# Kernel optimization log

Measured on AMD Instinct MI355X. Metric: run time of the kernel, lower is better.

The kernel has to match this reference:

```python
import jax, jax.numpy as jnp
import numpy as np

N_NODES = 100000
N_EDGES = 1600000
IN_DIM = 128
OUT_DIM = 64
NEG_SLOPE = 0.01  # torch F.leaky_relu default


def setup_inputs() -> dict:
    key = jax.random.key(0)
    k1, k2, k3, k4, k5 = jax.random.split(key, 5)
    h = jax.random.normal(k1, (N_NODES, IN_DIM), dtype=jnp.float32)
    src = jax.random.randint(k2, (N_EDGES,), 0, N_NODES, dtype=jnp.int32)
    dst = jax.random.randint(k3, (N_EDGES,), 0, N_NODES, dtype=jnp.int32)
    # xavier_normal with relu gain, as in reset_parameters
    gain = float(np.sqrt(2.0))
    fc_std = gain * np.sqrt(2.0 / (IN_DIM + OUT_DIM))
    at_std = gain * np.sqrt(2.0 / (2 * OUT_DIM + 1))
    fc_w = jax.random.normal(k4, (OUT_DIM, IN_DIM), dtype=jnp.float32) * fc_std
    attn_w = jax.random.normal(k5, (2 * OUT_DIM,), dtype=jnp.float32) * at_std
    return {"h": h, "src": src, "dst": dst, "fc_w": fc_w, "attn_w": attn_w}


def reference(h, src, dst, fc_w, attn_w):
    n = h.shape[0]
    d = fc_w.shape[0]
    z = h @ fc_w.T                                  # [N, D]
    # per-edge attention logit: attn_fc(concat(z_src, z_dst)) split into two dots
    a_src = z @ attn_w[:d]                          # [N]
    a_dst = z @ attn_w[d:]                          # [N]
    e = a_src[src] + a_dst[dst]                     # [E]
    e = jnp.where(e >= 0, e, NEG_SLOPE * e)         # leaky_relu
    # segment softmax over incoming edges of each dst node
    e_max = jax.ops.segment_max(e, dst, num_segments=n)   # [N]
    ex = jnp.exp(e - e_max[dst])                    # [E]
    denom = jax.ops.segment_sum(ex, dst, num_segments=n)  # [N]
    alpha = ex / denom[dst]                         # [E]
    # weighted scatter-sum of source features
    h_out = jax.ops.segment_sum(alpha[:, None] * z[src], dst, num_segments=n)
    return h_out
```

## Files before the change

kernel.cpp:

```cpp
#include <hip/hip_runtime.h>

#define D 64
#define IN 128
#define NEG_SLOPE 0.01f

#define NSLICE 32
#define SUBPS  32
#define NSUB   1024
#define EPB_A  3328
#define EPT_A  13
#define HALF   49
#define CAP2   1152
#define CAP_S  53248
#define CAP_SUB 2304

using f32x4  = __attribute__((ext_vector_type(4))) float;
using bf16x8 = __attribute__((ext_vector_type(8))) short;
using u16x8  = __attribute__((ext_vector_type(8))) unsigned short;

__device__ __forceinline__ short f2bf(float f) {
    unsigned u = __float_as_uint(f);
    u = u + 0x7FFFu + ((u >> 16) & 1u);
    return (short)(u >> 16);
}
__device__ __forceinline__ float bf2f(unsigned short u) {
    return __uint_as_float((unsigned)u << 16);
}
__device__ __forceinline__ int mdiv(int n, unsigned M) {
    return (int)__umulhi((unsigned)n, M);
}

__global__ __launch_bounds__(256) void k_partA_proj(
    const int* __restrict__ src, const int* __restrict__ dst,
    int* __restrict__ slice_cur, int* __restrict__ partA,
    int n_edges, int nps1, unsigned M1, int n_partA,
    const float* __restrict__ h, const float* __restrict__ fc_w,
    const float* __restrict__ attn_w,
    unsigned short* __restrict__ zb, float* __restrict__ a_src, float* __restrict__ a_dst,
    int n_nodes)
{
    __shared__ int smem[4352];

    if (blockIdx.x < n_partA) {
        int* loff  = smem;
        int* lbase = smem + 40;
        int* lcur  = smem + 80;
        int* lsort = smem + 128;
        const int tid = threadIdx.x;
        const int e0 = blockIdx.x * EPB_A;
        const int e1 = min(e0 + EPB_A, n_edges);

        if (tid < NSLICE) { loff[tid] = 0; lcur[tid] = 0; }
        __syncthreads();

        int myp[EPT_A], mysl[EPT_A];
        #pragma unroll
        for (int j = 0; j < EPT_A; ++j) {
            int i = e0 + j * 256 + tid;
            mysl[j] = -1;
            if (i < e1) {
                int d = dst[i], s = src[i];
                int sl = mdiv(d, M1);
                mysl[j] = sl;
                myp[j]  = s | ((d - sl * nps1) << 17);
                atomicAdd(&loff[sl], 1);
            }
        }
        __syncthreads();
        if (tid < NSLICE) {
            int v = loff[tid];
            int sc = v;
            #pragma unroll
            for (int o = 1; o < NSLICE; o <<= 1) {
                int t2 = __shfl_up(sc, o, 64);
                if (tid >= o) sc += t2;
            }
            loff[tid] = sc - v;
            if (tid == NSLICE - 1) loff[NSLICE] = sc;
        }
        __syncthreads();
        if (tid < NSLICE)
            lbase[tid] = tid * CAP_S + atomicAdd(&slice_cur[tid * 16], loff[tid + 1] - loff[tid]);
        #pragma unroll
        for (int j = 0; j < EPT_A; ++j)
            if (mysl[j] >= 0) {
                int r = atomicAdd(&lcur[mysl[j]], 1);
                lsort[loff[mysl[j]] + r] = myp[j];
            }
        __syncthreads();
        for (int s = 0; s < NSLICE; ++s) {
            int b = loff[s], e = loff[s + 1], gb = lbase[s];
            int lim = (s + 1) * CAP_S;
            for (int i = b + tid; i < e; i += 256) {
                int pos = gb + (i - b);
                if (pos < lim) partA[pos] = lsort[i];
            }
        }
        return;
    }

    float* zst = (float*)smem;
    const int wid  = threadIdx.x >> 6;
    const int lane = threadIdx.x & 63;
    const int g16  = lane >> 4;
    const int l16  = lane & 15;

    bf16x8 bfrag[4][4];
    #pragma unroll
    for (int t = 0; t < 4; ++t) {
        const float* wrow = fc_w + (size_t)(t * 16 + l16) * IN + g16 * 8;
        #pragma unroll
        for (int ks = 0; ks < 4; ++ks) {
            f32x4 w0 = *(const f32x4*)(wrow + ks * 32);
            f32x4 w1 = *(const f32x4*)(wrow + ks * 32 + 4);
            bf16x8 b;
            b[0] = f2bf(w0[0]); b[1] = f2bf(w0[1]); b[2] = f2bf(w0[2]); b[3] = f2bf(w0[3]);
            b[4] = f2bf(w1[0]); b[5] = f2bf(w1[1]); b[6] = f2bf(w1[2]); b[7] = f2bf(w1[3]);
            bfrag[t][ks] = b;
        }
    }

    float awx[4], awy[4];
    #pragma unroll
    for (int t = 0; t < 4; ++t) {
        awx[t] = attn_w[t * 16 + l16];
        awy[t] = attn_w[D + t * 16 + l16];
    }

    const int grp0 = (blockIdx.x - n_partA) * 16 + wid * 4;
    #pragma unroll
    for (int it = 0; it < 4; ++it) {
        const int gb = (grp0 + it) * 16;
        if (gb >= n_nodes) break;

        const float* hrow = h + (size_t)(gb + l16) * IN + g16 * 8;
        bf16x8 afrag[4];
        #pragma unroll
        for (int ks = 0; ks < 4; ++ks) {
            f32x4 h0 = *(const f32x4*)(hrow + ks * 32);
            f32x4 h1 = *(const f32x4*)(hrow + ks * 32 + 4);
            bf16x8 a;
            a[0] = f2bf(h0[0]); a[1] = f2bf(h0[1]); a[2] = f2bf(h0[2]); a[3] = f2bf(h0[3]);
            a[4] = f2bf(h1[0]); a[5] = f2bf(h1[1]); a[6] = f2bf(h1[2]); a[7] = f2bf(h1[3]);
            afrag[ks] = a;
        }

        f32x4 acc[4] = {f32x4{0,0,0,0}, f32x4{0,0,0,0}, f32x4{0,0,0,0}, f32x4{0,0,0,0}};
        #pragma unroll
        for (int t = 0; t < 4; ++t)
            #pragma unroll
            for (int ks = 0; ks < 4; ++ks)
                acc[t] = __builtin_amdgcn_mfma_f32_16x16x32_bf16(
                    afrag[ks], bfrag[t][ks], acc[t], 0, 0, 0);

        #pragma unroll
        for (int t = 0; t < 4; ++t)
            #pragma unroll
            for (int r = 0; r < 4; ++r)
                zst[wid * 1088 + (g16 * 4 + r) * 68 + t * 16 + l16] = acc[t][r];

        const int rrow = lane >> 2;
        const int rcol = (lane & 3) * 16;
        const float* zr0 = &zst[wid * 1088 + rrow * 68 + rcol];
        f32x4 v0 = *(const f32x4*)(zr0);
        f32x4 v1 = *(const f32x4*)(zr0 + 4);
        f32x4 v2 = *(const f32x4*)(zr0 + 8);
        f32x4 v3 = *(const f32x4*)(zr0 + 12);
        u16x8 p0, p1;
        p0[0] = (unsigned short)f2bf(v0[0]); p0[1] = (unsigned short)f2bf(v0[1]);
        p0[2] = (unsigned short)f2bf(v0[2]); p0[3] = (unsigned short)f2bf(v0[3]);
        p0[4] = (unsigned short)f2bf(v1[0]); p0[5] = (unsigned short)f2bf(v1[1]);
        p0[6] = (unsigned short)f2bf(v1[2]); p0[7] = (unsigned short)f2bf(v1[3]);
        p1[0] = (unsigned short)f2bf(v2[0]); p1[1] = (unsigned short)f2bf(v2[1]);
        p1[2] = (unsigned short)f2bf(v2[2]); p1[3] = (unsigned short)f2bf(v2[3]);
        p1[4] = (unsigned short)f2bf(v3[0]); p1[5] = (unsigned short)f2bf(v3[1]);
        p1[6] = (unsigned short)f2bf(v3[2]); p1[7] = (unsigned short)f2bf(v3[3]);
        *(u16x8*)&zb[(size_t)(gb + rrow) * D + rcol]     = p0;
        *(u16x8*)&zb[(size_t)(gb + rrow) * D + rcol + 8] = p1;

        #pragma unroll
        for (int r = 0; r < 4; ++r) {
            float as = acc[0][r] * awx[0] + acc[1][r] * awx[1]
                     + acc[2][r] * awx[2] + acc[3][r] * awx[3];
            float ad = acc[0][r] * awy[0] + acc[1][r] * awy[1]
                     + acc[2][r] * awy[2] + acc[3][r] * awy[3];
            #pragma unroll
            for (int o = 1; o < 16; o <<= 1) {
                as += __shfl_xor(as, o, 64);
                ad += __shfl_xor(ad, o, 64);
            }
            if (l16 == 0) {
                a_src[gb + g16 * 4 + r] = as;
                a_dst[gb + g16 * 4 + r] = ad;
            }
        }
    }
}

__global__ __launch_bounds__(256) void k_partB(
    const int* __restrict__ partA, const int* __restrict__ slice_cur,
    int* __restrict__ sub_cur, int* __restrict__ part2, int nps2, unsigned M2)
{
    __shared__ int loff[SUBPS + 1], lbase[SUBPS], lcur[SUBPS];
    __shared__ int lsort[2048];
    const int tid   = threadIdx.x;
    const int slice = blockIdx.x >> 5;
    const int bid   = blockIdx.x & 31;
    const int s0   = slice * CAP_S;
    const int cntS = min(slice_cur[slice * 16], CAP_S);
    const int chunk = (cntS + 31) >> 5;
    int c0 = s0 + bid * chunk;
    int c1 = min(c0 + chunk, s0 + cntS);

    for (int r0 = c0; r0 < c1; r0 += 2048) {
        int r1 = min(r0 + 2048, c1);
        if (tid < SUBPS) { loff[tid] = 0; lcur[tid] = 0; }
        __syncthreads();
        int myp[8], mysb[8];
        #pragma unroll
        for (int j = 0; j < 8; ++j) {
            int i = r0 + j * 256 + tid;
            mysb[j] = -1;
            if (i < r1) {
                int p = partA[i];
                int dloc = p >> 17;
                int sb = mdiv(dloc, M2);
                mysb[j] = sb;
                myp[j]  = (p & 0x1FFFF) | ((dloc - sb * nps2) << 17);
                atomicAdd(&loff[sb], 1);
            }
        }
        __syncthreads();
        if (tid < SUBPS) {
            int v = loff[tid];
            int sc = v;
            #pragma unroll
            for (int o = 1; o < SUBPS; o <<= 1) {
                int t2 = __shfl_up(sc, o, 64);
                if (tid >= o) sc += t2;
            }
            loff[tid] = sc - v;
            if (tid == SUBPS - 1) loff[SUBPS] = sc;
        }
        __syncthreads();
        if (tid < SUBPS) {
            int sub = slice * SUBPS + tid;
            lbase[tid] = sub * CAP_SUB + atomicAdd(&sub_cur[sub], loff[tid + 1] - loff[tid]);
        }
        #pragma unroll
        for (int j = 0; j < 8; ++j)
            if (mysb[j] >= 0) {
                int r = atomicAdd(&lcur[mysb[j]], 1);
                lsort[loff[mysb[j]] + r] = myp[j];
            }
        __syncthreads();
        for (int s = 0; s < SUBPS; ++s) {
            int b = loff[s], e = loff[s + 1], gb = lbase[s];
            int lim = (slice * SUBPS + s + 1) * CAP_SUB;
            for (int i = b + tid; i < e; i += 256) {
                int pos = gb + (i - b);
                if (pos < lim) part2[pos] = lsort[i];
            }
        }
        __syncthreads();
    }
}

__global__ __launch_bounds__(256) void k_fused(
    const int* __restrict__ part2, const int* __restrict__ sub_cur,
    const float* __restrict__ a_src, const float* __restrict__ a_dst,
    const u16x8* __restrict__ zb8, float4* __restrict__ out4,
    int n_nodes, int nps2)
{
    __shared__ int   sdeg[56], scur[56];
    __shared__ float sden[56];
    __shared__ int   soff[65];
    __shared__ int   sstage[CAP_SUB];
    __shared__ int2  sedge[CAP2];

    const int tid  = threadIdx.x;
    const int sub  = blockIdx.x >> 1;
    const int half = blockIdx.x & 1;
    const int nb0  = sub * nps2;
    if (nb0 >= n_nodes) return;
    const int nn   = min(nps2, n_nodes - nb0);
    const int lo   = half * HALF;
    const int hi   = min(nn, lo + HALF);
    const int nloc = hi - lo;
    if (nloc <= 0) return;
    const int s0  = sub * CAP_SUB;
    const int cnt = min(sub_cur[sub], CAP_SUB);

    for (int i = tid; i < 56; i += 256) { sdeg[i] = 0; scur[i] = 0; sden[i] = 0.f; }
    __syncthreads();

    for (int i = tid; i < cnt; i += 256) {
        int p = part2[s0 + i];
        sstage[i] = p;
        int local = p >> 17;
        if (local >= lo && local < hi) atomicAdd(&sdeg[local - lo], 1);
    }
    __syncthreads();

    if (tid < 64) {
        int v = (tid < nloc) ? sdeg[tid] : 0;
        int sc = v;
        #pragma unroll
        for (int o = 1; o < 64; o <<= 1) {
            int t2 = __shfl_up(sc, o, 64);
            if (tid >= o) sc += t2;
        }
        soff[tid + 1] = sc;
        if (tid == 0) soff[0] = 0;
    }
    __syncthreads();

    const bool fits = (soff[nloc] <= CAP2);

    if (fits) {
        for (int i = tid; i < cnt; i += 256) {
            int p = sstage[i];
            int local = p >> 17;
            if (local >= lo && local < hi) {
                int l2 = local - lo;
                int s = p & 0x1FFFF;
                int pos = soff[l2] + atomicAdd(&scur[l2], 1);
                float e = a_src[s] + a_dst[nb0 + local];
                e = (e >= 0.f) ? e : NEG_SLOPE * e;
                float ex = __expf(e);
                sedge[pos] = make_int2(s << 3, __float_as_int(ex));
                atomicAdd(&sden[l2], ex);
            }
        }
    }
    __syncthreads();

    if (fits) {
        const int group = tid >> 3;
        const int l8    = tid & 7;
        for (int n = group; n < nloc; n += 32) {
            int beg = soff[n], deg = sdeg[n];
            f32x4 a0 = {0.f,0.f,0.f,0.f}, a1 = {0.f,0.f,0.f,0.f};
            for (int i = 0; i < deg; ++i) {
                int2 me = sedge[beg + i];
                float w = __int_as_float(me.y);
                u16x8 zr = zb8[(size_t)me.x + l8];
                a0[0] = fmaf(w, bf2f(zr[0]), a0[0]);
                a0[1] = fmaf(w, bf2f(zr[1]), a0[1]);
                a0[2] = fmaf(w, bf2f(zr[2]), a0[2]);
                a0[3] = fmaf(w, bf2f(zr[3]), a0[3]);
                a1[0] = fmaf(w, bf2f(zr[4]), a1[0]);
                a1[1] = fmaf(w, bf2f(zr[5]), a1[1]);
                a1[2] = fmaf(w, bf2f(zr[6]), a1[2]);
                a1[3] = fmaf(w, bf2f(zr[7]), a1[3]);
            }
            float inv = (deg > 0) ? 1.f / sden[n] : 0.f;
            out4[(size_t)(nb0 + lo + n) * 16 + l8 * 2] =
                make_float4(a0[0] * inv, a0[1] * inv, a0[2] * inv, a0[3] * inv);
            out4[(size_t)(nb0 + lo + n) * 16 + l8 * 2 + 1] =
                make_float4(a1[0] * inv, a1[1] * inv, a1[2] * inv, a1[3] * inv);
        }
    } else {
        const ushort4* zb4 = (const ushort4*)zb8;
        const int wave = tid >> 6, lane = tid & 63, l16 = lane & 15;
        for (int n = wave; n < nloc; n += 4) {
            int deg = 0;
            float adn = a_dst[nb0 + lo + n];
            float dsum = 0.f;
            float4 acc = make_float4(0.f, 0.f, 0.f, 0.f);
            for (int c = 0; c < cnt; c += 64) {
                int j = c + lane;
                float ex = 0.f;
                if (j < cnt) {
                    int p = sstage[j];
                    if ((p >> 17) == lo + n) {
                        float e = a_src[p & 0x1FFFF] + adn;
                        e = (e >= 0.f) ? e : NEG_SLOPE * e;
                        ex = __expf(e);
                        ++deg;
                    }
                }
                float exs = ex;
                #pragma unroll
                for (int o = 32; o > 0; o >>= 1) exs += __shfl_xor(exs, o, 64);
                dsum += exs;
            }
            #pragma unroll
            for (int o = 32; o > 0; o >>= 1) deg += __shfl_xor(deg, o, 64);
            for (int j = 0; j < cnt; ++j) {
                int p = sstage[j];
                if ((p >> 17) == lo + n) {
                    int s = p & 0x1FFFF;
                    float e = a_src[s] + adn;
                    e = (e >= 0.f) ? e : NEG_SLOPE * e;
                    float w = __expf(e);
                    if (lane < 16) {
                        ushort4 zr = zb4[(size_t)(s << 4) + l16];
                        acc.x = fmaf(w, bf2f(zr.x), acc.x);
                        acc.y = fmaf(w, bf2f(zr.y), acc.y);
                        acc.z = fmaf(w, bf2f(zr.z), acc.z);
                        acc.w = fmaf(w, bf2f(zr.w), acc.w);
                    }
                }
            }
            #pragma unroll
            for (int o = 16; o <= 32; o <<= 1) {
                acc.x += __shfl_xor(acc.x, o, 64);
                acc.y += __shfl_xor(acc.y, o, 64);
                acc.z += __shfl_xor(acc.z, o, 64);
                acc.w += __shfl_xor(acc.w, o, 64);
            }
            if (lane < 16) {
                float inv = (deg > 0) ? 1.f / dsum : 0.f;
                out4[(size_t)(nb0 + lo + n) * 16 + l16] =
                    make_float4(acc.x * inv, acc.y * inv, acc.z * inv, acc.w * inv);
            }
        }
    }
}

extern "C" void kernel_launch(void* const* d_in, const int* in_sizes, int n_in,
                              void* d_out, int out_size, void* d_ws, size_t ws_size,
                              hipStream_t stream) {
    const float* h      = (const float*)d_in[0];
    const int*   src    = (const int*)d_in[1];
    const int*   dst    = (const int*)d_in[2];
    const float* fc_w   = (const float*)d_in[3];
    const float* attn_w = (const float*)d_in[4];

    const int n_nodes = in_sizes[0] / IN;
    const int n_edges = in_sizes[1];
    float* out = (float*)d_out;

    const int nps2 = (n_nodes + NSUB - 1) / NSUB;
    const int nps1 = nps2 * SUBPS;
    const int nba  = (n_edges + EPB_A - 1) / EPB_A;
    const int n_proj = (n_nodes + 255) / 256;
    const unsigned M1 = (unsigned)((0x100000000ULL + nps1 - 1) / (unsigned)nps1);
    const unsigned M2 = (unsigned)((0x100000000ULL + nps2 - 1) / (unsigned)nps2);

    char* p = (char*)d_ws;
    unsigned short* zb = (unsigned short*)p; p += (size_t)n_nodes * D * sizeof(unsigned short);
    int*   partA     = (int*)p;   p += (size_t)NSLICE * CAP_S * sizeof(int);
    int*   part2     = (int*)p;   p += (size_t)NSUB * CAP_SUB * sizeof(int);
    float* a_src     = (float*)p; p += (size_t)n_nodes * sizeof(float);
    float* a_dst     = (float*)p; p += (size_t)n_nodes * sizeof(float);
    int*   slice_cur = (int*)p;   p += NSLICE * 16 * sizeof(int);
    int*   sub_cur   = (int*)p;   p += NSUB * sizeof(int);

    hipMemsetAsync(slice_cur, 0, (NSLICE * 16 + NSUB) * sizeof(int), stream);

    k_partA_proj<<<dim3(nba + n_proj), dim3(256), 0, stream>>>(
        src, dst, slice_cur, partA, n_edges, nps1, M1, nba,
        h, fc_w, attn_w, zb, a_src, a_dst, n_nodes);
    k_partB<<<dim3(NSLICE * 32), dim3(256), 0, stream>>>(
        partA, slice_cur, sub_cur, part2, nps2, M2);
    k_fused<<<dim3(NSUB * 2), dim3(256), 0, stream>>>(
        part2, sub_cur, a_src, a_dst, (const u16x8*)zb, (float4*)out, n_nodes, nps2);
}
```

Baseline: 95.57 us.

## Move projection GEMM to run alongside second partition pass; vectorize first pass loads

The node projection blocks are now co-launched with the second-level bucketing pass instead of the first-level pass, so the first partition kernel runs alone with smaller 2048-edge blocks. Those blocks load src/dst with int4 vector loads. The aim is better load balance between the two bucketing passes and the projection work, and fewer, wider memory transactions for the edge reads. More blocks in the first pass means more global atomics on the slice counters.

```diff
diff --git a/kernel.cpp b/kernel.cpp
--- a/kernel.cpp
+++ b/kernel.cpp
@@ -7,8 +7,7 @@
 #define NSLICE 32
 #define SUBPS  32
 #define NSUB   1024
-#define EPB_A  3328
-#define EPT_A  13
+#define EPB_A  2048
 #define HALF   49
 #define CAP2   1152
 #define CAP_S  53248
@@ -30,10 +29,80 @@
     return (int)__umulhi((unsigned)n, M);
 }
 
-__global__ __launch_bounds__(256) void k_partA_proj(
+__global__ __launch_bounds__(256) void k_partA(
     const int* __restrict__ src, const int* __restrict__ dst,
     int* __restrict__ slice_cur, int* __restrict__ partA,
-    int n_edges, int nps1, unsigned M1, int n_partA,
+    int n_edges, int nps1, unsigned M1)
+{
+    __shared__ int loff[NSLICE + 1], lbase[NSLICE], lcur[NSLICE];
+    __shared__ int lsort[EPB_A];
+    const int tid = threadIdx.x;
+    const int e0 = blockIdx.x * EPB_A;
+    const int e1 = min(e0 + EPB_A, n_edges);
+
+    if (tid < NSLICE) { loff[tid] = 0; lcur[tid] = 0; }
+    __syncthreads();
+
+    const int4* dst4 = (const int4*)dst;
+    const int4* src4 = (const int4*)src;
+    int myp[8], mysl[8];
+    #pragma unroll
+    for (int c = 0; c < 2; ++c) {
+        int b4 = (e0 >> 2) + c * 256 + tid;
+        bool v4 = (b4 * 4 < e1);
+        int4 d4 = v4 ? dst4[b4] : make_int4(0, 0, 0, 0);
+        int4 s4 = v4 ? src4[b4] : make_int4(0, 0, 0, 0);
+        const int* dp = (const int*)&d4;
+        const int* sp = (const int*)&s4;
+        #pragma unroll
+        for (int k = 0; k < 4; ++k) {
+            int j = c * 4 + k;
+            mysl[j] = -1;
+            int idx = b4 * 4 + k;
+            if (v4 && idx < e1) {
+                int d = dp[k], s = sp[k];
+                int sl = mdiv(d, M1);
+                mysl[j] = sl;
+                myp[j]  = s | ((d - sl * nps1) << 17);
+                atomicAdd(&loff[sl], 1);
+            }
+        }
+    }
+    __syncthreads();
+    if (tid < NSLICE) {
+        int v = loff[tid];
+        int sc = v;
+        #pragma unroll
+        for (int o = 1; o < NSLICE; o <<= 1) {
+            int t2 = __shfl_up(sc, o, 64);
+            if (tid >= o) sc += t2;
+        }
+        loff[tid] = sc - v;
+        if (tid == NSLICE - 1) loff[NSLICE] = sc;
+    }
+    __syncthreads();
+    if (tid < NSLICE)
+        lbase[tid] = tid * CAP_S + atomicAdd(&slice_cur[tid * 16], loff[tid + 1] - loff[tid]);
+    #pragma unroll
+    for (int j = 0; j < 8; ++j)
+        if (mysl[j] >= 0) {
+            int r = atomicAdd(&lcur[mysl[j]], 1);
+            lsort[loff[mysl[j]] + r] = myp[j];
+        }
+    __syncthreads();
+    for (int s = 0; s < NSLICE; ++s) {
+        int b = loff[s], e = loff[s + 1], gb = lbase[s];
+        int lim = (s + 1) * CAP_S;
+        for (int i = b + tid; i < e; i += 256) {
+            int pos = gb + (i - b);
+            if (pos < lim) partA[pos] = lsort[i];
+        }
+    }
+}
+
+__global__ __launch_bounds__(256) void k_partB_proj(
+    const int* __restrict__ partA, const int* __restrict__ slice_cur,
+    int* __restrict__ sub_cur, int* __restrict__ part2, int nps2, unsigned M2,
     const float* __restrict__ h, const float* __restrict__ fc_w,
     const float* __restrict__ attn_w,
     unsigned short* __restrict__ zb, float* __restrict__ a_src, float* __restrict__ a_dst,
@@ -41,60 +110,71 @@
 {
     __shared__ int smem[4352];
 
-    if (blockIdx.x < n_partA) {
+    if (blockIdx.x < NSUB) {
         int* loff  = smem;
         int* lbase = smem + 40;
         int* lcur  = smem + 80;
         int* lsort = smem + 128;
-        const int tid = threadIdx.x;
-        const int e0 = blockIdx.x * EPB_A;
-        const int e1 = min(e0 + EPB_A, n_edges);
-
-        if (tid < NSLICE) { loff[tid] = 0; lcur[tid] = 0; }
-        __syncthreads();
-
-        int myp[EPT_A], mysl[EPT_A];
-        #pragma unroll
-        for (int j = 0; j < EPT_A; ++j) {
-            int i = e0 + j * 256 + tid;
-            mysl[j] = -1;
-            if (i < e1) {
-                int d = dst[i], s = src[i];
-                int sl = mdiv(d, M1);
-                mysl[j] = sl;
-                myp[j]  = s | ((d - sl * nps1) << 17);
-                atomicAdd(&loff[sl], 1);
-            }
-        }
-        __syncthreads();
-        if (tid < NSLICE) {
-            int v = loff[tid];
-            int sc = v;
-            #pragma unroll
-            for (int o = 1; o < NSLICE; o <<= 1) {
-                int t2 = __shfl_up(sc, o, 64);
-                if (tid >= o) sc += t2;
-            }
-            loff[tid] = sc - v;
-            if (tid == NSLICE - 1) loff[NSLICE] = sc;
-        }
-        __syncthreads();
-        if (tid < NSLICE)
-            lbase[tid] = tid * CAP_S + atomicAdd(&slice_cur[tid * 16], loff[tid + 1] - loff[tid]);
-        #pragma unroll
-        for (int j = 0; j < EPT_A; ++j)
-            if (mysl[j] >= 0) {
-                int r = atomicAdd(&lcur[mysl[j]], 1);
-                lsort[loff[mysl[j]] + r] = myp[j];
-            }
-        __syncthreads();
-        for (int s = 0; s < NSLICE; ++s) {
-            int b = loff[s], e = loff[s + 1], gb = lbase[s];
-            int lim = (s + 1) * CAP_S;
-            for (int i = b + tid; i < e; i += 256) {
-                int pos = gb + (i - b);
-                if (pos < lim) partA[pos] = lsort[i];
-            }
+        const int tid   = threadIdx.x;
+        const int slice = blockIdx.x >> 5;
+        const int bid   = blockIdx.x & 31;
+        const int s0   = slice * CAP_S;
+        const int cntS = min(slice_cur[slice * 16], CAP_S);
+        const int chunk = (cntS + 31) >> 5;
+        int c0 = s0 + bid * chunk;
+        int c1 = min(c0 + chunk, s0 + cntS);
+
+        for (int r0 = c0; r0 < c1; r0 += 2048) {
+            int r1 = min(r0 + 2048, c1);
+            if (tid < SUBPS) { loff[tid] = 0; lcur[tid] = 0; }
+            __syncthreads();
+            int myp[8], mysb[8];
+            #pragma unroll
+            for (int j = 0; j < 8; ++j) {
+                int i = r0 + j * 256 + tid;
+                mysb[j] = -1;
+                if (i < r1) {
+                    int p = partA[i];
+                    int dloc = p >> 17;
+                    int sb = mdiv(dloc, M2);
+                    mysb[j] = sb;
+                    myp[j]  = (p & 0x1FFFF) | ((dloc - sb * nps2) << 17);
+                    atomicAdd(&loff[sb], 1);
+                }
+            }
+            __syncthreads();
+            if (tid < SUBPS) {
+                int v = loff[tid];
+                int sc = v;
+                #pragma unroll
+                for (int o = 1; o < SUBPS; o <<= 1) {
+                    int t2 = __shfl_up(sc, o, 64);
+                    if (tid >= o) sc += t2;
+                }
+                loff[tid] = sc - v;
+                if (tid == SUBPS - 1) loff[SUBPS] = sc;
+            }
+            __syncthreads();
+            if (tid < SUBPS) {
+                int sub = slice * SUBPS + tid;
+                lbase[tid] = sub * CAP_SUB + atomicAdd(&sub_cur[sub], loff[tid + 1] - loff[tid]);
+            }
+            #pragma unroll
+            for (int j = 0; j < 8; ++j)
+                if (mysb[j] >= 0) {
+                    int r = atomicAdd(&lcur[mysb[j]], 1);
+                    lsort[loff[mysb[j]] + r] = myp[j];
+                }
+            __syncthreads();
+            for (int s = 0; s < SUBPS; ++s) {
+                int b = loff[s], e = loff[s + 1], gb = lbase[s];
+                int lim = (slice * SUBPS + s + 1) * CAP_SUB;
+                for (int i = b + tid; i < e; i += 256) {
+                    int pos = gb + (i - b);
+                    if (pos < lim) part2[pos] = lsort[i];
+                }
+            }
+            __syncthreads();
         }
         return;
     }
@@ -127,7 +207,7 @@
         awy[t] = attn_w[D + t * 16 + l16];
     }
 
-    const int grp0 = (blockIdx.x - n_partA) * 16 + wid * 4;
+    const int grp0 = (blockIdx.x - NSUB) * 16 + wid * 4;
     #pragma unroll
     for (int it = 0; it < 4; ++it) {
         const int gb = (grp0 + it) * 16;
@@ -194,75 +274,6 @@
                 a_dst[gb + g16 * 4 + r] = ad;
             }
         }
-    }
-}
-
-__global__ __launch_bounds__(256) void k_partB(
-    const int* __restrict__ partA, const int* __restrict__ slice_cur,
-    int* __restrict__ sub_cur, int* __restrict__ part2, int nps2, unsigned M2)
-{
-    __shared__ int loff[SUBPS + 1], lbase[SUBPS], lcur[SUBPS];
-    __shared__ int lsort[2048];
-    const int tid   = threadIdx.x;
-    const int slice = blockIdx.x >> 5;
-    const int bid   = blockIdx.x & 31;
-    const int s0   = slice * CAP_S;
-    const int cntS = min(slice_cur[slice * 16], CAP_S);
-    const int chunk = (cntS + 31) >> 5;
-    int c0 = s0 + bid * chunk;
-    int c1 = min(c0 + chunk, s0 + cntS);
-
-    for (int r0 = c0; r0 < c1; r0 += 2048) {
-        int r1 = min(r0 + 2048, c1);
-        if (tid < SUBPS) { loff[tid] = 0; lcur[tid] = 0; }
-        __syncthreads();
-        int myp[8], mysb[8];
-        #pragma unroll
-        for (int j = 0; j < 8; ++j) {
-            int i = r0 + j * 256 + tid;
-            mysb[j] = -1;
-            if (i < r1) {
-                int p = partA[i];
-                int dloc = p >> 17;
-                int sb = mdiv(dloc, M2);
-                mysb[j] = sb;
-                myp[j]  = (p & 0x1FFFF) | ((dloc - sb * nps2) << 17);
-                atomicAdd(&loff[sb], 1);
-            }
-        }
-        __syncthreads();
-        if (tid < SUBPS) {
-            int v = loff[tid];
-            int sc = v;
-            #pragma unroll
-            for (int o = 1; o < SUBPS; o <<= 1) {
-                int t2 = __shfl_up(sc, o, 64);
-                if (tid >= o) sc += t2;
-            }
-            loff[tid] = sc - v;
-            if (tid == SUBPS - 1) loff[SUBPS] = sc;
-        }
-        __syncthreads();
-        if (tid < SUBPS) {
-            int sub = slice * SUBPS + tid;
-            lbase[tid] = sub * CAP_SUB + atomicAdd(&sub_cur[sub], loff[tid + 1] - loff[tid]);
-        }
-        #pragma unroll
-        for (int j = 0; j < 8; ++j)
-            if (mysb[j] >= 0) {
-                int r = atomicAdd(&lcur[mysb[j]], 1);
-                lsort[loff[mysb[j]] + r] = myp[j];
-            }
-        __syncthreads();
-        for (int s = 0; s < SUBPS; ++s) {
-            int b = loff[s], e = loff[s + 1], gb = lbase[s];
-            int lim = (slice * SUBPS + s + 1) * CAP_SUB;
-            for (int i = b + tid; i < e; i += 256) {
-                int pos = gb + (i - b);
-                if (pos < lim) part2[pos] = lsort[i];
-            }
-        }
-        __syncthreads();
     }
 }
 
@@ -450,11 +461,11 @@
 
     hipMemsetAsync(slice_cur, 0, (NSLICE * 16 + NSUB) * sizeof(int), stream);
 
-    k_partA_proj<<<dim3(nba + n_proj), dim3(256), 0, stream>>>(
-        src, dst, slice_cur, partA, n_edges, nps1, M1, nba,
+    k_partA<<<dim3(nba), dim3(256), 0, stream>>>(
+        src, dst, slice_cur, partA, n_edges, nps1, M1);
+    k_partB_proj<<<dim3(NSUB + n_proj), dim3(256), 0, stream>>>(
+        partA, slice_cur, sub_cur, part2, nps2, M2,
         h, fc_w, attn_w, zb, a_src, a_dst, n_nodes);
-    k_partB<<<dim3(NSLICE * 32), dim3(256), 0, stream>>>(
-        partA, slice_cur, sub_cur, part2, nps2, M2);
     k_fused<<<dim3(NSUB * 2), dim3(256), 0, stream>>>(
         part2, sub_cur, a_src, a_dst, (const u16x8*)zb, (float4*)out, n_nodes, nps2);
 }
```

Result: slower. 109.4 us (+14.5%).

## Store z in permuted column layout and stage weights in LDS

Applied to the files above, without the earlier changes.

The projection stage now stages bf16 weight fragments in shared memory instead of per-thread registers, and writes z straight from MFMA accumulators in a permuted column order. This removes the LDS transpose round-trip and may reduce register pressure, with launch bounds asking for higher occupancy. Because the permutation places logical column 4*l16+t at physical column t*16+l16, the aggregation kernel now un-permutes on output with strided float2/scalar stores instead of float4 stores. The cost is less coalesced output writes and extra LDS reads of weights per tile.

```diff
diff --git a/kernel.cpp b/kernel.cpp
--- a/kernel.cpp
+++ b/kernel.cpp
@@ -30,7 +30,8 @@
     return (int)__umulhi((unsigned)n, M);
 }
 
-__global__ __launch_bounds__(256) void k_partA_proj(
+
+__global__ __launch_bounds__(256, 8) void k_partA_proj(
     const int* __restrict__ src, const int* __restrict__ dst,
     int* __restrict__ slice_cur, int* __restrict__ partA,
     int n_edges, int nps1, unsigned M1, int n_partA,
@@ -39,7 +40,7 @@
     unsigned short* __restrict__ zb, float* __restrict__ a_src, float* __restrict__ a_dst,
     int n_nodes)
 {
-    __shared__ int smem[4352];
+    __shared__ int smem[4096];
 
     if (blockIdx.x < n_partA) {
         int* loff  = smem;
@@ -99,26 +100,29 @@
         return;
     }
 
-    float* zst = (float*)smem;
-    const int wid  = threadIdx.x >> 6;
-    const int lane = threadIdx.x & 63;
+    unsigned short* wlds = (unsigned short*)smem;
+    const int tid  = threadIdx.x;
+    const int wid  = tid >> 6;
+    const int lane = tid & 63;
     const int g16  = lane >> 4;
     const int l16  = lane & 15;
 
-    bf16x8 bfrag[4][4];
-    #pragma unroll
-    for (int t = 0; t < 4; ++t) {
-        const float* wrow = fc_w + (size_t)(t * 16 + l16) * IN + g16 * 8;
-        #pragma unroll
-        for (int ks = 0; ks < 4; ++ks) {
-            f32x4 w0 = *(const f32x4*)(wrow + ks * 32);
-            f32x4 w1 = *(const f32x4*)(wrow + ks * 32 + 4);
-            bf16x8 b;
-            b[0] = f2bf(w0[0]); b[1] = f2bf(w0[1]); b[2] = f2bf(w0[2]); b[3] = f2bf(w0[3]);
-            b[4] = f2bf(w1[0]); b[5] = f2bf(w1[1]); b[6] = f2bf(w1[2]); b[7] = f2bf(w1[3]);
-            bfrag[t][ks] = b;
-        }
-    }
+    for (int c = tid; c < 1024; c += 256) {
+        int row = c >> 4;
+        int cb  = (c & 15) * 8;
+        const float* wp = fc_w + (size_t)row * IN + cb;
+        f32x4 w0 = *(const f32x4*)(wp);
+        f32x4 w1 = *(const f32x4*)(wp + 4);
+        int t   = row >> 4, lv = row & 15;
+        int ks  = cb >> 5,  gv = (cb >> 3) & 3;
+        u16x8 b;
+        b[0] = (unsigned short)f2bf(w0[0]); b[1] = (unsigned short)f2bf(w0[1]);
+        b[2] = (unsigned short)f2bf(w0[2]); b[3] = (unsigned short)f2bf(w0[3]);
+        b[4] = (unsigned short)f2bf(w1[0]); b[5] = (unsigned short)f2bf(w1[1]);
+        b[6] = (unsigned short)f2bf(w1[2]); b[7] = (unsigned short)f2bf(w1[3]);
+        *(u16x8*)&wlds[(size_t)(((t * 4 + ks) * 4 + gv) * 16 + lv) * 8] = b;
+    }
+    __syncthreads();
 
     float awx[4], awy[4];
     #pragma unroll
@@ -149,34 +153,20 @@
         #pragma unroll
         for (int t = 0; t < 4; ++t)
             #pragma unroll
-            for (int ks = 0; ks < 4; ++ks)
-                acc[t] = __builtin_amdgcn_mfma_f32_16x16x32_bf16(
-                    afrag[ks], bfrag[t][ks], acc[t], 0, 0, 0);
-
-        #pragma unroll
-        for (int t = 0; t < 4; ++t)
-            #pragma unroll
-            for (int r = 0; r < 4; ++r)
-                zst[wid * 1088 + (g16 * 4 + r) * 68 + t * 16 + l16] = acc[t][r];
-
-        const int rrow = lane >> 2;
-        const int rcol = (lane & 3) * 16;
-        const float* zr0 = &zst[wid * 1088 + rrow * 68 + rcol];
-        f32x4 v0 = *(const f32x4*)(zr0);
-        f32x4 v1 = *(const f32x4*)(zr0 + 4);
-        f32x4 v2 = *(const f32x4*)(zr0 + 8);
-        f32x4 v3 = *(const f32x4*)(zr0 + 12);
-        u16x8 p0, p1;
-        p0[0] = (unsigned short)f2bf(v0[0]); p0[1] = (unsigned short)f2bf(v0[1]);
-        p0[2] = (unsigned short)f2bf(v0[2]); p0[3] = (unsigned short)f2bf(v0[3]);
-        p0[4] = (unsigned short)f2bf(v1[0]); p0[5] = (unsigned short)f2bf(v1[1]);
-        p0[6] = (unsigned short)f2bf(v1[2]); p0[7] = (unsigned short)f2bf(v1[3]);
-        p1[0] = (unsigned short)f2bf(v2[0]); p1[1] = (unsigned short)f2bf(v2[1]);
-        p1[2] = (unsigned short)f2bf(v2[2]); p1[3] = (unsigned short)f2bf(v2[3]);
-        p1[4] = (unsigned short)f2bf(v3[0]); p1[5] = (unsigned short)f2bf(v3[1]);
-        p1[6] = (unsigned short)f2bf(v3[2]); p1[7] = (unsigned short)f2bf(v3[3]);
-        *(u16x8*)&zb[(size_t)(gb + rrow) * D + rcol]     = p0;
-        *(u16x8*)&zb[(size_t)(gb + rrow) * D + rcol + 8] = p1;
+            for (int ks = 0; ks < 4; ++ks) {
+                bf16x8 b = *(const bf16x8*)&wlds[(size_t)(((t * 4 + ks) * 4 + g16) * 16 + l16) * 8];
+                acc[t] = __builtin_amdgcn_mfma_f32_16x16x32_bf16(afrag[ks], b, acc[t], 0, 0, 0);
+            }
+
+        #pragma unroll
+        for (int r = 0; r < 4; ++r) {
+            ushort4 st;
+            st.x = (unsigned short)f2bf(acc[0][r]);
+            st.y = (unsigned short)f2bf(acc[1][r]);
+            st.z = (unsigned short)f2bf(acc[2][r]);
+            st.w = (unsigned short)f2bf(acc[3][r]);
+            *(ushort4*)&zb[(size_t)(gb + g16 * 4 + r) * D + l16 * 4] = st;
+        }
 
         #pragma unroll
         for (int r = 0; r < 4; ++r) {
@@ -269,7 +259,7 @@
 __global__ __launch_bounds__(256) void k_fused(
     const int* __restrict__ part2, const int* __restrict__ sub_cur,
     const float* __restrict__ a_src, const float* __restrict__ a_dst,
-    const u16x8* __restrict__ zb8, float4* __restrict__ out4,
+    const u16x8* __restrict__ zb8, float* __restrict__ out,
     int n_nodes, int nps2)
 {
     __shared__ int   sdeg[56], scur[56];
@@ -355,10 +345,11 @@
                 a1[3] = fmaf(w, bf2f(zr[7]), a1[3]);
             }
             float inv = (deg > 0) ? 1.f / sden[n] : 0.f;
-            out4[(size_t)(nb0 + lo + n) * 16 + l8 * 2] =
-                make_float4(a0[0] * inv, a0[1] * inv, a0[2] * inv, a0[3] * inv);
-            out4[(size_t)(nb0 + lo + n) * 16 + l8 * 2 + 1] =
-                make_float4(a1[0] * inv, a1[1] * inv, a1[2] * inv, a1[3] * inv);
+            float* op = out + (size_t)(nb0 + lo + n) * D + 2 * l8;
+            *(float2*)(op)      = make_float2(a0[0] * inv, a1[0] * inv);
+            *(float2*)(op + 16) = make_float2(a0[1] * inv, a1[1] * inv);
+            *(float2*)(op + 32) = make_float2(a0[2] * inv, a1[2] * inv);
+            *(float2*)(op + 48) = make_float2(a0[3] * inv, a1[3] * inv);
         }
     } else {
         const ushort4* zb4 = (const ushort4*)zb8;
@@ -412,8 +403,11 @@
             }
             if (lane < 16) {
                 float inv = (deg > 0) ? 1.f / dsum : 0.f;
-                out4[(size_t)(nb0 + lo + n) * 16 + l16] =
-                    make_float4(acc.x * inv, acc.y * inv, acc.z * inv, acc.w * inv);
+                float* op = out + (size_t)(nb0 + lo + n) * D + l16;
+                op[0]  = acc.x * inv;
+                op[16] = acc.y * inv;
+                op[32] = acc.z * inv;
+                op[48] = acc.w * inv;
             }
         }
     }
@@ -456,5 +450,5 @@
     k_partB<<<dim3(NSLICE * 32), dim3(256), 0, stream>>>(
         partA, slice_cur, sub_cur, part2, nps2, M2);
     k_fused<<<dim3(NSUB * 2), dim3(256), 0, stream>>>(
-        part2, sub_cur, a_src, a_dst, (const u16x8*)zb, (float4*)out, n_nodes, nps2);
-}
+        part2, sub_cur, a_src, a_dst, (const u16x8*)zb, out, n_nodes, nps2);
+}
```

After: 84.88 us (median of 2 runs). 11.2% less time.
